# Optimization experiments

Hardware: AMD Instinct MI355X
Metric: run time of the kernel (lower is better)

The kernel has to match this reference:

```python
import jax, jax.numpy as jnp
import numpy as np

B, C, K, V, S = 16384, 1024, 128, 256, 6
HM, HG, M = 512, 384, 1024
LB = 2
GATE_DIM = C + K + 2 * V + 5  # 1669
CADENCE = 8.0
TEMP = 0.25
REFRESH_T, SPAWN_T, PROMOTE_T, RETIRE_T = 0.55, 0.60, 0.50, 0.15
DECAY = 0.995
EPS_N = 1e-6


def _mlp(x, W1, b1, W2, b2):
    return jax.nn.gelu(x @ W1 + b1, approximate=False) @ W2 + b2


def _l2norm(x):
    n = jnp.linalg.norm(x, axis=-1, keepdims=True)
    return x / jnp.maximum(n, EPS_N)


def setup_inputs():
    key = jax.random.key(0)
    ks = jax.random.split(key, 16)
    p = lambda k, sh: (0.02 * jax.random.normal(k, sh)).astype(jnp.float32)
    return {
        "context": jax.random.normal(ks[0], (B, C), jnp.float32),
        "ledger_bias": jax.random.normal(ks[1], (B, LB), jnp.float32),
        "keys": jax.random.normal(ks[2], (B, S, K), jnp.float32),
        "values": jax.random.normal(ks[3], (B, S, V), jnp.float32),
        "confidence": jax.random.uniform(ks[4], (B, S, 1), jnp.float32),
        "age": 16.0 * jax.random.uniform(ks[5], (B, S, 1), jnp.float32),
        "alive": (jax.random.uniform(ks[6], (B, S, 1)) > 0.3).astype(jnp.float32),
        "Wk1": p(ks[7], (C, HM)), "bk1": jnp.zeros(HM, jnp.float32),
        "Wk2": p(ks[8], (HM, K)), "bk2": jnp.zeros(K, jnp.float32),
        "Wv1": p(ks[9], (C, HM)), "bv1": jnp.zeros(HM, jnp.float32),
        "Wv2": p(ks[10], (HM, V)), "bv2": jnp.zeros(V, jnp.float32),
        "Wg1": p(ks[11], (4, GATE_DIM, HG)), "bg1": jnp.zeros((4, HG), jnp.float32),
        "Wg2": p(ks[12], (4, HG, 1)), "bg2": jnp.zeros((4, 1), jnp.float32),
        "Wsum": p(ks[13], (V, M)), "bsum": jnp.zeros(M, jnp.float32),
        "g_ln": jnp.ones(M, jnp.float32), "b_ln": jnp.zeros(M, jnp.float32),
    }


def _forward(context, ledger_bias, keys, values, confidence, age, alive,
             Wk1, bk1, Wk2, bk2, Wv1, bv1, Wv2, bv2,
             Wg1, bg1, Wg2, bg2, Wsum, bsum, g_ln, b_ln):
    cand_key = _l2norm(_mlp(context, Wk1, bk1, Wk2, bk2))   # [B,K]
    cand_val = _mlp(context, Wv1, bv1, Wv2, bv2)            # [B,V]
    # --- slot match: cosine similarity over live slots, gather best ---
    live = alive[..., 0] > 0                                # [B,S]
    safe_keys = _l2norm(keys + (1.0 - alive) * 1e-4)
    scores = jnp.einsum("bd,bsd->bs", cand_key, safe_keys)
    scores = jnp.where(live, scores, -1e4)
    has_live = jnp.any(live, axis=1, keepdims=True)         # [B,1]
    best_score = jnp.where(has_live, scores.max(axis=1, keepdims=True), 0.0)
    best_index = jnp.where(has_live, jnp.argmax(scores, axis=1, keepdims=True), 0)
    matched_val = jnp.take_along_axis(values, best_index[:, :, None], axis=1)[:, 0]
    matched_age = jnp.take_along_axis(age, best_index[:, :, None], axis=1)[:, 0]
    cadence_prior = jax.nn.sigmoid((matched_age - CADENCE) / CADENCE)
    surprise = 1.0 - best_score
    feats = jnp.concatenate([context, cand_key, cand_val, matched_val,
                             best_score, cadence_prior, surprise, ledger_bias], axis=-1)
    # --- four gate MLPs fused into one batched einsum ---
    h = jax.nn.gelu(jnp.einsum("bf,gfh->bgh", feats, Wg1) + bg1, approximate=False)
    probs = jax.nn.sigmoid(jnp.einsum("bgh,gho->bgo", h, Wg2) + bg2)[:, :, 0]  # [B,4]
    refresh_p, spawn_p, promote_p, retire_p = (probs[:, i:i + 1] for i in range(4))
    # --- soft masks (hard=False path) ---
    has_live_f = alive.max(axis=1)                          # [B,1]
    t = max(TEMP, 1e-4)
    refresh_raw = jax.nn.sigmoid((refresh_p - REFRESH_T) / t) * has_live_f
    spawn_raw = jax.nn.sigmoid((spawn_p - SPAWN_T) / t)
    denom = 1.0 + refresh_raw + spawn_raw
    refresh = refresh_raw / denom
    spawn = spawn_raw / denom
    promote = jax.nn.sigmoid((promote_p - PROMOTE_T) / t)
    retire = jax.nn.sigmoid((retire_p - RETIRE_T) / t)
    # --- spawn slot selection ---
    inactive = (alive[..., 0] < 0.5).astype(jnp.float32)
    has_inactive = inactive.max(axis=1, keepdims=True) > 0.5
    inactive_choice = jnp.argmax(inactive, axis=1, keepdims=True)
    utility = (confidence - 0.01 * age)[..., 0]
    utility = jnp.where(best_index == jnp.arange(S)[None, :], 1e4, utility)
    spawn_index = jnp.where(has_inactive, inactive_choice,
                            jnp.argmin(utility, axis=1, keepdims=True))
    # --- masked scatter update into slot memory ---
    match_hot = jax.nn.one_hot(best_index[:, 0], S, dtype=keys.dtype)[:, :, None]
    spawn_hot = jax.nn.one_hot(spawn_index[:, 0], S, dtype=keys.dtype)[:, :, None]
    refresh_slot = match_hot * refresh[:, None, :]
    spawn_slot = spawn_hot * spawn[:, None, :]
    retire_slot = match_hot * retire[:, None, :]
    write = jnp.clip(refresh_slot + spawn_slot, 0.0, 1.0)
    keys_n = keys * (1.0 - write) + write * cand_key[:, None, :]
    values_n = values * (1.0 - write) + write * cand_val[:, None, :]
    conf_n = (confidence * DECAY * (1.0 - write) + write) * (1.0 - retire_slot)
    age_n = (age + alive) * (1.0 - write)
    alive_n = jnp.clip(alive * (1.0 - retire_slot) + write, 0.0, 1.0)
    # --- confidence-weighted summary + promoted memory token ---
    w = alive_n * conf_n
    summary = (values_n * w).sum(axis=1) / (w.sum(axis=1) + EPS_N)  # [B,V]
    z = summary @ Wsum + bsum
    mu = z.mean(axis=-1, keepdims=True)
    var = ((z - mu) ** 2).mean(axis=-1, keepdims=True)
    promoted = promote * (((z - mu) / jnp.sqrt(var + 1e-5)) * g_ln + b_ln)
    return promoted, summary, keys_n, values_n, conf_n, age_n, alive_n


def reference(context, ledger_bias, keys, values, confidence, age, alive,
              Wk1, bk1, Wk2, bk2, Wv1, bv1, Wv2, bv2,
              Wg1, bg1, Wg2, bg2, Wsum, bsum, g_ln, b_ln):
    return _forward(context, ledger_bias, keys, values, confidence, age, alive,
                    Wk1, bk1, Wk2, bk2, Wv1, bv1, Wv2, bv2,
                    Wg1, bg1, Wg2, bg2, Wsum, bsum, g_ln, b_ln)
```

## Files before the change

kernel.cpp:

```cpp
#include <hip/hip_runtime.h>
#include <math.h>

static constexpr int Bsz  = 16384;
static constexpr int Cdim = 1024;
static constexpr int Kdim = 128;
static constexpr int Vdim = 256;
static constexpr int HMd  = 512;
static constexpr int GOUTd= 1536;
static constexpr int GDIM = 1669;
static constexpr int GPAD = 1728;
static constexpr int F2D  = 704;
static constexpr int Mdim = 1024;
static constexpr float TAU = 2e-3f;

typedef __attribute__((ext_vector_type(8))) _Float16 f16x8;
typedef __attribute__((ext_vector_type(4))) _Float16 f16x4;
typedef __attribute__((ext_vector_type(4))) float f32x4;

__device__ __forceinline__ float sigm(float x){ return 1.0f/(1.0f+__expf(-x)); }
__device__ __forceinline__ float gelu(float x){
    float y = 0.70710678118654752440f * x;
    float a = fabsf(y);
    float t1 = __builtin_amdgcn_rcpf(fmaf(0.3275911f, a, 1.0f));
    float p = t1*fmaf(t1, fmaf(t1, fmaf(t1, fmaf(t1, 1.061405429f, -1.453152027f),
                                         1.421413741f), -0.284496736f), 0.254829592f);
    float e = __expf(-a*a);
    float er = fmaf(-p, e, 1.0f);
    er = (y < 0.0f) ? -er : er;
    return 0.5f*x*(1.0f+er);
}
__device__ __forceinline__ ushort f2h(float f){
    return __builtin_bit_cast(ushort, (_Float16)f);
}


__global__ __launch_bounds__(256) void k_zero(int* p){ if (threadIdx.x==0) *p = 0; }

__global__ __launch_bounds__(256) void k_cat(float* __restrict__ dst,
        const float* __restrict__ a, const float* __restrict__ b, int na, int ntot){
    int i = blockIdx.x*256 + threadIdx.x;
    if (i >= ntot) return;
    dst[i] = (i < na) ? a[i] : b[i-na];
}

__global__ __launch_bounds__(256) void k_wt(const float* __restrict__ W,
                                            ushort* __restrict__ Wt, int K, int N){
    __shared__ float tile[64][65];
    int n0 = blockIdx.x*64, k0 = blockIdx.y*64;
    int tx = threadIdx.x & 63, ty = threadIdx.x >> 6;
    #pragma unroll
    for (int i=0;i<64;i+=4)
        tile[ty+i][tx] = W[(size_t)(k0+ty+i)*N + n0 + tx];
    __syncthreads();
    #pragma unroll
    for (int i=0;i<64;i+=4)
        Wt[(size_t)(n0+ty+i)*K + k0 + tx] = f2h(tile[tx][ty+i]);
}

__global__ __launch_bounds__(256) void k_wg1t(const float* __restrict__ Wg1,
                                              ushort* __restrict__ Wt){
    __shared__ float tile[64][65];
    int g = blockIdx.z;
    int h0 = blockIdx.x*64, f0 = blockIdx.y*64;
    int tx = threadIdx.x & 63, ty = threadIdx.x >> 6;
    #pragma unroll
    for (int i=0;i<64;i+=4){
        int f = f0+ty+i;
        tile[ty+i][tx] = (f < GDIM) ? Wg1[((size_t)g*GDIM+f)*384 + h0+tx] : 0.0f;
    }
    __syncthreads();
    #pragma unroll
    for (int i=0;i<64;i+=4)
        Wt[((size_t)(g*384 + h0+ty+i))*GPAD + f0+tx] = f2h(tile[tx][ty+i]);
}

__global__ __launch_bounds__(256) void k_cvt(const float* __restrict__ x,
                                             ushort* __restrict__ y, size_t n4){
    size_t i = (size_t)blockIdx.x*256 + threadIdx.x;
    if (i >= n4) return;
    float4 v = ((const float4*)x)[i];
    ushort4 o = { f2h(v.x), f2h(v.y), f2h(v.z), f2h(v.w) };
    ((ushort4*)y)[i] = o;
}

__device__ __forceinline__ void gload_lds16(const void* g, void* l){
    typedef __attribute__((address_space(1))) const unsigned gu32;
    typedef __attribute__((address_space(3))) unsigned lu32;
    __builtin_amdgcn_global_load_lds((gu32*)(unsigned long long)g,
                                     (lu32*)(unsigned)(unsigned long long)l,
                                     16, 0, 0);
}

template<int ACT, int OUTM, int SRC, int NX>
__global__ __launch_bounds__(512, 4) void k_mgemm(const ushort* __restrict__ A,
        const ushort* __restrict__ A2, const ushort* __restrict__ Bt,
        const float* __restrict__ bias, const float* __restrict__ Wg2,
        void* __restrict__ Cout, int K, int lda){
    __shared__ alignas(16) ushort lds[24576];
    ushort* As = lds;
    ushort* Bs = lds + 16384;
    int t = threadIdx.x;
    int l = t & 63, wv = t >> 6;
    int wrow = wv >> 1, wcol = wv & 1;
    int nwg = NX * (int)gridDim.y;
    int orig = (int)blockIdx.y * NX + (int)blockIdx.x;
    int qq = nwg >> 3, rr = nwg & 7;
    int xcd = orig & 7, loc = orig >> 3;
    int wgid = (xcd < rr ? xcd*(qq+1) : rr*(qq+1) + (xcd-rr)*qq) + loc;
    int bx = wgid % NX;
    int by = wgid / NX;
    size_t row0 = (size_t)by * 256;
    int col0 = bx * 128;
    constexpr int N = NX*128;
    f32x4 acc[4][4] = {};
    int lrow = l >> 3;
    int lc8  = (l & 7) ^ lrow;

    for (int k0 = 0; k0 < K; k0 += 64){
        const ushort* Ag; size_t astr; int koff;
        if (SRC == 1){
            if (k0 < 1024){ Ag = A;  astr = 1024; koff = k0; }
            else          { Ag = A2; astr = F2D;  koff = k0 - 1024; }
        } else if (SRC == 2){
            Ag = A; astr = (size_t)lda; koff = k0 + (bx ? 512 : 0);
        } else { Ag = A; astr = (size_t)lda; koff = k0; }
        #pragma unroll
        for (int i = 0; i < 4; ++i){
            int ch = wv*4 + i;
            int r  = ch*8 + lrow;
            gload_lds16(Ag + (row0 + r)*astr + koff + lc8*8, As + ch*512);
        }
        #pragma unroll
        for (int i = 0; i < 2; ++i){
            int ch = wv*2 + i;
            int r  = ch*8 + lrow;
            gload_lds16(Bt + (size_t)(col0 + r)*K + k0 + lc8*8, Bs + ch*512);
        }
        __syncthreads();
        #pragma unroll
        for (int kk = 0; kk < 2; ++kk){
            f16x8 af[4], bfr[4];
            int j8 = kk*4 + (l >> 4);
            #pragma unroll
            for (int m = 0; m < 4; ++m){
                int row = wrow*64 + m*16 + (l & 15);
                int c16 = j8 ^ (row & 7);
                af[m] = *(const f16x8*)(const void*)(As + row*64 + c16*8);
            }
            #pragma unroll
            for (int n = 0; n < 4; ++n){
                int rowb = wcol*64 + n*16 + (l & 15);
                int c16 = j8 ^ (rowb & 7);
                bfr[n] = *(const f16x8*)(const void*)(Bs + rowb*64 + c16*8);
            }
            #pragma unroll
            for (int m = 0; m < 4; ++m)
                #pragma unroll
                for (int n = 0; n < 4; ++n)
                    acc[m][n] = __builtin_amdgcn_mfma_f32_16x16x32_f16(af[m], bfr[n], acc[m][n], 0, 0, 0);
        }
        __syncthreads();
    }
    int q = l >> 4, cf = l & 15;
    if (OUTM == 2){
        float* sacc = (float*)lds;
        if (t < 256) sacc[t] = 0.f;
        __syncthreads();
        #pragma unroll
        for (int m = 0; m < 4; ++m){
            #pragma unroll
            for (int i = 0; i < 4; ++i){
                float v = 0.f;
                #pragma unroll
                for (int n = 0; n < 4; ++n){
                    int col = col0 + wcol*64 + n*16 + cf;
                    float z = acc[m][n][i] + bias[col];
                    v += gelu(z) * Wg2[col];
                }
                atomicAdd(&sacc[wrow*64 + m*16 + q*4 + i], v);
            }
        }
        __syncthreads();
        if (t < 256) ((float*)Cout)[(row0 + t)*NX + bx] = sacc[t];
    } else {
        #pragma unroll
        for (int m = 0; m < 4; ++m){
            #pragma unroll
            for (int n = 0; n < 4; ++n){
                int col = col0 + wcol*64 + n*16 + cf;
                float bv = bias[col];
                #pragma unroll
                for (int i = 0; i < 4; ++i){
                    size_t r = row0 + wrow*64 + m*16 + q*4 + i;
                    float v = acc[m][n][i] + bv;
                    if (ACT == 1) v = gelu(v);
                    if (OUTM == 1) ((ushort*)Cout)[r*N + col] = f2h(v);
                    else           ((float*) Cout)[r*N + col] = v;
                }
            }
        }
    }
}

template<int ACT>
__global__ __launch_bounds__(256) void k_gemm_dyn(const float* __restrict__ A,
                                                  const float* __restrict__ W,
                                                  const float* __restrict__ bias,
                                                  float* __restrict__ C,
                                                  const int* __restrict__ cntp,
                                                  int N, int K){
    int M = (*cntp + 63) & ~63;
    size_t row0 = (size_t)blockIdx.y * 64;
    if ((int)row0 >= M) return;
    __shared__ float As[32][68];
    __shared__ float Ws[32][64];
    int t  = threadIdx.x;
    int tx = t & 15, ty = t >> 4;
    int col0 = blockIdx.x * 64;
    float acc[4][4] = {};
    int ra = t >> 3;
    int ca = (t & 7) << 2;
    int rw = t >> 4;
    int cw = (t & 15) << 2;
    for (int k0 = 0; k0 < K; k0 += 32){
        float4 a0 = *(const float4*)(A + (row0 + ra)*K + k0 + ca);
        float4 a1 = *(const float4*)(A + (row0 + ra + 32)*K + k0 + ca);
        float4 w0 = *(const float4*)(W + (size_t)(k0 + rw)*N + col0 + cw);
        float4 w1 = *(const float4*)(W + (size_t)(k0 + rw + 16)*N + col0 + cw);
        As[ca+0][ra] = a0.x; As[ca+1][ra] = a0.y; As[ca+2][ra] = a0.z; As[ca+3][ra] = a0.w;
        As[ca+0][ra+32] = a1.x; As[ca+1][ra+32] = a1.y; As[ca+2][ra+32] = a1.z; As[ca+3][ra+32] = a1.w;
        *(float4*)&Ws[rw][cw]    = w0;
        *(float4*)&Ws[rw+16][cw] = w1;
        __syncthreads();
        #pragma unroll
        for (int kk = 0; kk < 32; ++kk){
            float4 av = *(const float4*)&As[kk][ty*4];
            float4 wv = *(const float4*)&Ws[kk][tx*4];
            float a4[4] = {av.x, av.y, av.z, av.w};
            float w4[4] = {wv.x, wv.y, wv.z, wv.w};
            #pragma unroll
            for (int i=0;i<4;i++)
                #pragma unroll
                for (int j=0;j<4;j++)
                    acc[i][j] = fmaf(a4[i], w4[j], acc[i][j]);
        }
        __syncthreads();
    }
    #pragma unroll
    for (int i=0;i<4;i++){
        size_t r = row0 + ty*4 + i;
        #pragma unroll
        for (int j=0;j<4;j++){
            int c = col0 + tx*4 + j;
            float v = acc[i][j] + bias[c];
            if (ACT == 1) v = gelu(v);
            C[r*N + c] = v;
        }
    }
}

__global__ __launch_bounds__(256) void k_gather(const float* __restrict__ ctx,
        const int* __restrict__ flaglist, const int* __restrict__ flagcnt,
        float* __restrict__ fctx, int b0){
    int i = (blockIdx.x<<2) + (threadIdx.x>>6);
    int lane = threadIdx.x & 63;
    int cnt = *flagcnt;
    int cntpad = (cnt + 63) & ~63;
    if (i >= cntpad) return;
    float4* dst = (float4*)(fctx + (size_t)i*1024);
    if (i < cnt){
        const float4* src = (const float4*)(ctx + ((size_t)b0 + flaglist[i])*1024);
        #pragma unroll
        for (int j=0;j<4;j++) dst[lane + 64*j] = src[lane + 64*j];
    } else {
        float4 z = {0.f,0.f,0.f,0.f};
        #pragma unroll
        for (int j=0;j<4;j++) dst[lane + 64*j] = z;
    }
}

__global__ __launch_bounds__(256) void k_fixapply(const float* __restrict__ fck,
        const float* __restrict__ keys, const float* __restrict__ values,
        const float* __restrict__ age,  const float* __restrict__ alive,
        float* __restrict__ ckc, ushort* __restrict__ feats2, int* __restrict__ bidx,
        const int* __restrict__ flagcnt, const int* __restrict__ flaglist, int b0){
    int i = (blockIdx.x<<2) + (threadIdx.x>>6);
    int lane = threadIdx.x & 63;
    if (i >= *flagcnt) return;
    int w = flaglist[i];
    size_t b = (size_t)b0 + w;
    float2 c2 = ((const float2*)(fck + (size_t)i*128))[lane];
    float ss = c2.x*c2.x + c2.y*c2.y;
    #pragma unroll
    for (int o=32;o;o>>=1) ss += __shfl_xor(ss,o);
    float inv = 1.0f / fmaxf(sqrtf(ss), 1e-6f);
    float2 cc; cc.x = c2.x*inv; cc.y = c2.y*inv;
    ((float2*)(ckc + (size_t)w*128))[lane] = cc;
    ushort* f2 = feats2 + (size_t)w*F2D;
    { ushort2 o = { f2h(cc.x), f2h(cc.y) };
      ((ushort2*)f2)[lane] = o; }
    float s1v = -1e30f; int bi = 0; int anylive = 0;
    #pragma unroll
    for (int s=0;s<6;s++){
        float a = alive[b*6+s];
        float2 k2 = ((const float2*)(keys + (b*6+s)*128))[lane];
        float ks = k2.x*k2.x + k2.y*k2.y;
        float dt = cc.x*k2.x + cc.y*k2.y;
        #pragma unroll
        for (int o=32;o;o>>=1){ ks += __shfl_xor(ks,o); dt += __shfl_xor(dt,o); }
        float sc;
        if (a > 0.0f){ sc = dt / fmaxf(sqrtf(ks), 1e-6f); anylive = 1; }
        else sc = -1e4f;
        if (sc > s1v){ s1v = sc; bi = s; }
    }
    int bis = anylive ? bi : 0;
    float bsc = anylive ? s1v : 0.0f;
    float4 mv = ((const float4*)(values + (b*6+bis)*256))[lane];
    ushort4 mo = { f2h(mv.x), f2h(mv.y), f2h(mv.z), f2h(mv.w) };
    ((ushort4*)(f2+384))[lane] = mo;
    if (lane == 0){
        bidx[w] = bis;
        float mage = age[b*6 + bis];
        f2[640] = f2h(bsc);
        f2[641] = f2h(sigm((mage - 8.0f)*0.125f));
        f2[642] = f2h(1.0f - bsc);
    }
}

__global__ __launch_bounds__(256) void k_feats(
        const float* __restrict__ ledger, const float* __restrict__ keys,
        const float* __restrict__ values, const float* __restrict__ age,
        const float* __restrict__ alive,  const float* __restrict__ ckv,
        float* __restrict__ ckc, ushort* __restrict__ feats2,
        int* __restrict__ bidx, int* __restrict__ flagcnt, int* __restrict__ flaglist,
        int b0){
    int w = (blockIdx.x<<2) + (threadIdx.x>>6);
    int lane = threadIdx.x & 63;
    size_t b = (size_t)b0 + w;
    const float* ckr = ckv + (size_t)w*384;
    float2 cr2 = ((const float2*)ckr)[lane];
    float ssc = cr2.x*cr2.x + cr2.y*cr2.y;
    #pragma unroll
    for (int o=32;o;o>>=1) ssc += __shfl_xor(ssc,o);
    float invc = 1.0f / fmaxf(sqrtf(ssc), 1e-6f);
    float2 cc; cc.x = cr2.x*invc; cc.y = cr2.y*invc;
    ((float2*)(ckc + (size_t)w*128))[lane] = cc;
    float s1v = -1e30f, s2v = -1e30f; int bi = 0; int anylive = 0;
    #pragma unroll
    for (int s=0;s<6;s++){
        float a = alive[b*6+s];
        float2 k2 = ((const float2*)(keys + (b*6+s)*128))[lane];
        float ss = k2.x*k2.x + k2.y*k2.y;
        float dt = cc.x*k2.x + cc.y*k2.y;
        #pragma unroll
        for (int o=32;o;o>>=1){ ss += __shfl_xor(ss,o); dt += __shfl_xor(dt,o); }
        float sc;
        if (a > 0.0f){ sc = dt / fmaxf(sqrtf(ss), 1e-6f); anylive = 1; }
        else sc = -1e4f;
        if (sc > s1v){ s2v = s1v; s1v = sc; bi = s; }
        else if (sc > s2v) s2v = sc;
    }
    float best_score = anylive ? s1v : 0.0f;
    int bis = anylive ? bi : 0;
    if (lane == 0 && (s1v - s2v) < TAU){
        int pos = atomicAdd(flagcnt, 1);
        flaglist[pos] = w;
    }
    float4 mv = ((const float4*)(values + (b*6+bis)*256))[lane];
    float mage = age[b*6+bis];
    float cad = sigm((mage - 8.0f)*0.125f);
    ushort* f2 = feats2 + (size_t)w*F2D;
    { ushort2 o = { f2h(cc.x), f2h(cc.y) };
      ((ushort2*)f2)[lane] = o; }
    { float4 v = ((const float4*)(ckr+128))[lane];
      ushort4 o = { f2h(v.x), f2h(v.y), f2h(v.z), f2h(v.w) };
      ((ushort4*)(f2+128))[lane] = o; }
    { ushort4 o = { f2h(mv.x), f2h(mv.y), f2h(mv.z), f2h(mv.w) };
      ((ushort4*)(f2+384))[lane] = o; }
    if (lane == 0){
        f2[640] = f2h(best_score);
        f2[641] = f2h(cad);
        f2[642] = f2h(1.0f - best_score);
        f2[643] = f2h(ledger[b*2]);
        f2[644] = f2h(ledger[b*2+1]);
        bidx[w] = bis;
    }
    if (lane < GPAD - GDIM) f2[645+lane] = 0;
}

__global__ __launch_bounds__(256) void k_update(const float* __restrict__ keys,
        const float* __restrict__ values, const float* __restrict__ conf,
        const float* __restrict__ age,    const float* __restrict__ alive,
        const float* __restrict__ ckC,    const float* __restrict__ ckv,
        const float* __restrict__ part,   const float* __restrict__ bg2,
        const int* __restrict__ bidx,
        float* __restrict__ probsC,
        float* __restrict__ o_keys, float* __restrict__ o_vals,
        float* __restrict__ o_conf, float* __restrict__ o_age,
        float* __restrict__ o_aliv, float* __restrict__ o_sum,
        ushort* __restrict__ o_sumb, int b0){
    int w = (blockIdx.x<<2) + (threadIdx.x>>6);
    int lane = threadIdx.x & 63;
    size_t b = (size_t)b0 + w;
    const float* pp = part + (size_t)w*12;
    float pb[4];
    #pragma unroll
    for (int g=0; g<4; ++g)
        pb[g] = sigm(pp[3*g] + pp[3*g+1] + pp[3*g+2] + bg2[g]);
    if (lane < 4) probsC[w*4 + lane] = pb[lane];
    float rp = pb[0], sp = pb[1], tp = pb[3];
    float al[6], cf[6], ag[6];
    float hl = 0.f;
    #pragma unroll
    for (int s=0;s<6;s++){
        al[s]=alive[b*6+s]; cf[s]=conf[b*6+s]; ag[s]=age[b*6+s];
        hl = fmaxf(hl, al[s]);
    }
    float rr = hl * sigm((rp-0.55f)*4.0f);
    float sr = sigm((sp-0.60f)*4.0f);
    float den = 1.0f + rr + sr;
    float refresh = rr/den, spawn = sr/den;
    float retire = sigm((tp-0.15f)*4.0f);
    int bi = bidx[w];
    int ic = -1;
    #pragma unroll
    for (int s=5;s>=0;s--) if (al[s] < 0.5f) ic = s;
    int si;
    if (ic >= 0) si = ic;
    else {
        float bu = 1e30f; int am = 0;
        #pragma unroll
        for (int s=0;s<6;s++){
            float u = (s == bi) ? 1e4f : (cf[s] - 0.01f*ag[s]);
            if (u < bu){ bu = u; am = s; }
        }
        si = am;
    }
    float2 cc  = ((const float2*)(ckC + (size_t)w*128))[lane];
    float4 cvv = ((const float4*)(ckv + (size_t)w*384 + 128))[lane];
    float s0=0,s1=0,s2=0,s3=0, wsum=0;
    #pragma unroll
    for (int s=0;s<6;s++){
        float wr = refresh*(s==bi ? 1.0f:0.0f) + spawn*(s==si ? 1.0f:0.0f);
        wr = fminf(wr, 1.0f);
        float rs = (s==bi) ? retire : 0.0f;
        float om = 1.0f - wr;
        float2 k2 = ((const float2*)(keys + (b*6+s)*128))[lane];
        float2 kn; kn.x = k2.x*om + wr*cc.x; kn.y = k2.y*om + wr*cc.y;
        ((float2*)(o_keys + (b*6+s)*128))[lane] = kn;
        float4 vv = ((const float4*)(values + (b*6+s)*256))[lane];
        float4 vn;
        vn.x = vv.x*om + wr*cvv.x; vn.y = vv.y*om + wr*cvv.y;
        vn.z = vv.z*om + wr*cvv.z; vn.w = vv.w*om + wr*cvv.w;
        ((float4*)(o_vals + (b*6+s)*256))[lane] = vn;
        float cn  = (cf[s]*0.995f*om + wr) * (1.0f - rs);
        float an  = fminf(fmaxf(al[s]*(1.0f - rs) + wr, 0.0f), 1.0f);
        float agn = (ag[s] + al[s]) * om;
        float wgt = an * cn;
        wsum += wgt;
        s0 += vn.x*wgt; s1 += vn.y*wgt; s2 += vn.z*wgt; s3 += vn.w*wgt;
        if (lane == s){ o_conf[b*6+s] = cn; o_age[b*6+s] = agn; o_aliv[b*6+s] = an; }
    }
    float inv = 1.0f/(wsum + 1e-6f);
    float4 sm; sm.x = s0*inv; sm.y = s1*inv; sm.z = s2*inv; sm.w = s3*inv;
    ((float4*)(o_sum + b*256))[lane] = sm;
    ushort4 sb = { f2h(sm.x), f2h(sm.y), f2h(sm.z), f2h(sm.w) };
    ((ushort4*)(o_sumb + (size_t)w*256))[lane] = sb;
}

__global__ __launch_bounds__(256) void k_ln(const ushort* __restrict__ z,
        const float* __restrict__ probs, const float* __restrict__ g_ln,
        const float* __restrict__ b_ln,  float* __restrict__ o_prom, int b0){
    int w = blockIdx.x; int t = threadIdx.x;
    int lane = t & 63, wid = t >> 6;
    f16x4 hv = ((const f16x4*)(z + (size_t)w*1024))[t];
    float v0 = (float)hv[0], v1 = (float)hv[1], v2 = (float)hv[2], v3 = (float)hv[3];
    float s = v0+v1+v2+v3;
    #pragma unroll
    for (int o=32;o;o>>=1) s += __shfl_xor(s,o);
    __shared__ float red[4];
    if (lane==0) red[wid] = s;
    __syncthreads();
    float mu = (red[0]+red[1]+red[2]+red[3]) * (1.0f/1024.0f);
    float d0=v0-mu, d1=v1-mu, d2=v2-mu, d3=v3-mu;
    float ss = d0*d0+d1*d1+d2*d2+d3*d3;
    #pragma unroll
    for (int o=32;o;o>>=1) ss += __shfl_xor(ss,o);
    __syncthreads();
    if (lane==0) red[wid] = ss;
    __syncthreads();
    float var = (red[0]+red[1]+red[2]+red[3]) * (1.0f/1024.0f);
    float rstd = 1.0f / sqrtf(var + 1e-5f);
    float pm = sigm((probs[w*4+2]-0.50f)*4.0f);
    float4 g  = ((const float4*)g_ln)[t];
    float4 bb = ((const float4*)b_ln)[t];
    float4 o;
    o.x = pm*(d0*rstd*g.x + bb.x);
    o.y = pm*(d1*rstd*g.y + bb.y);
    o.z = pm*(d2*rstd*g.z + bb.z);
    o.w = pm*(d3*rstd*g.w + bb.w);
    ((float4*)(o_prom + ((size_t)b0 + w)*1024))[t] = o;
}

extern "C" void kernel_launch(void* const* d_in, const int* in_sizes, int n_in,
                              void* d_out, int out_size, void* d_ws, size_t ws_size,
                              hipStream_t stream){
    const float* ctx    = (const float*)d_in[0];
    const float* ledger = (const float*)d_in[1];
    const float* keys   = (const float*)d_in[2];
    const float* values = (const float*)d_in[3];
    const float* conf   = (const float*)d_in[4];
    const float* age    = (const float*)d_in[5];
    const float* alive  = (const float*)d_in[6];
    const float* Wk1 = (const float*)d_in[7];  const float* bk1 = (const float*)d_in[8];
    const float* Wk2 = (const float*)d_in[9];  const float* bk2 = (const float*)d_in[10];
    const float* Wv1 = (const float*)d_in[11]; const float* bv1 = (const float*)d_in[12];
    const float* Wv2 = (const float*)d_in[13]; const float* bv2 = (const float*)d_in[14];
    const float* Wg1 = (const float*)d_in[15]; const float* bg1 = (const float*)d_in[16];
    const float* Wg2 = (const float*)d_in[17]; const float* bg2 = (const float*)d_in[18];
    const float* Wsum= (const float*)d_in[19]; const float* bsum= (const float*)d_in[20];
    const float* g_ln= (const float*)d_in[21]; const float* b_ln= (const float*)d_in[22];

    float* out   = (float*)d_out;
    float* o_prom= out;
    float* o_sum = o_prom + (size_t)Bsz*Mdim;
    float* o_keys= o_sum  + (size_t)Bsz*Vdim;
    float* o_vals= o_keys + (size_t)Bsz*6*Kdim;
    float* o_conf= o_vals + (size_t)Bsz*6*Vdim;
    float* o_age = o_conf + (size_t)Bsz*6;
    float* o_aliv= o_age  + (size_t)Bsz*6;

    char* p = (char*)d_ws;
    auto alloc = [&](size_t bytes)->char*{
        char* r = p; p += (bytes + 255) & ~(size_t)255; return r;
    };
    ushort* ctxh  = (ushort*)alloc((size_t)Bsz*Cdim*2);
    ushort* W1m   = (ushort*)alloc((size_t)1024*Cdim*2);
    ushort* W2m   = (ushort*)alloc((size_t)384*HMd*2);
    ushort* Wg1tt = (ushort*)alloc((size_t)GOUTd*GPAD*2);
    ushort* Wsumt = (ushort*)alloc((size_t)Mdim*Vdim*2);
    float*  biasm1= (float*) alloc(1024*4);
    float*  biasm2= (float*) alloc(384*4);
    size_t fixed = (size_t)(p - (char*)d_ws);
    size_t per_row = 2048 + 1536 + 512 + 1408 + 48 + 4096 + 512 + 16
                   + 4 + 4 + 2048 + 512 + 128;
    int CB = 16384;
    while (CB > 256 && fixed + (size_t)CB*per_row + 16384 > ws_size) CB >>= 1;
    ushort* H      = (ushort*)alloc((size_t)CB*1024*2);
    float*  ckv    = (float*) alloc((size_t)CB*384*4);
    float*  ckc    = (float*) alloc((size_t)CB*Kdim*4);
    ushort* feats2 = (ushort*)alloc((size_t)CB*F2D*2);
    float*  part   = (float*) alloc((size_t)CB*12*4);
    float*  zbuf   = (float*) alloc((size_t)CB*Mdim*4);
    ushort* sumb   = (ushort*)alloc((size_t)CB*Vdim*2);
    float*  probsC = (float*) alloc((size_t)CB*4*4);
    int*    bidxC  = (int*)   alloc((size_t)CB*4);
    int*    flagl  = (int*)   alloc((size_t)CB*4);
    int*    flagc  = (int*)   alloc(256);
    float*  fH     = (float*) alloc((size_t)CB*HMd*4);
    float*  fck    = (float*) alloc((size_t)CB*Kdim*4);
    float*  fctx   = zbuf;
    ushort* zh     = (ushort*)zbuf;

    dim3 blk(256);
    dim3 blk512(512);
    k_cvt<<<(int)(((size_t)Bsz*Cdim/4 + 255)/256), blk, 0, stream>>>(ctx, ctxh, (size_t)Bsz*Cdim/4);
    k_wt<<<dim3(HMd/64,  Cdim/64), blk, 0, stream>>>(Wk1, W1m,             Cdim, HMd);
    k_wt<<<dim3(HMd/64,  Cdim/64), blk, 0, stream>>>(Wv1, W1m + 512*Cdim,  Cdim, HMd);
    k_wt<<<dim3(Kdim/64, HMd/64),  blk, 0, stream>>>(Wk2, W2m,             HMd, Kdim);
    k_wt<<<dim3(Vdim/64, HMd/64),  blk, 0, stream>>>(Wv2, W2m + 128*HMd,   HMd, Vdim);
    k_wt<<<dim3(Mdim/64, Vdim/64), blk, 0, stream>>>(Wsum, Wsumt, Vdim, Mdim);
    k_wg1t<<<dim3(384/64, GPAD/64, 4), blk, 0, stream>>>(Wg1, Wg1tt);
    k_cat<<<(1024+255)/256, blk, 0, stream>>>(biasm1, bk1, bv1, 512, 1024);
    k_cat<<<(384+255)/256,  blk, 0, stream>>>(biasm2, bk2, bv2, 128, 384);

    for (int b0 = 0; b0 < Bsz; b0 += CB){
        k_zero<<<1, blk, 0, stream>>>(flagc);
        k_mgemm<1,1,0,8><<<dim3(8, CB/256), blk512, 0, stream>>>(
            ctxh + (size_t)b0*Cdim, nullptr, W1m, biasm1, nullptr, H, Cdim, Cdim);
        k_mgemm<0,0,2,3><<<dim3(3, CB/256), blk512, 0, stream>>>(
            H, nullptr, W2m, biasm2, nullptr, ckv, HMd, 1024);
        k_feats<<<CB/4, blk, 0, stream>>>(ledger, keys, values, age, alive,
                                          ckv, ckc, feats2, bidxC, flagc, flagl, b0);
        k_gather<<<CB/4, blk, 0, stream>>>(ctx, flagl, flagc, fctx, b0);
        k_gemm_dyn<1><<<dim3(HMd/64,  CB/64), blk, 0, stream>>>(fctx, Wk1, bk1, fH,  flagc, HMd,  Cdim);
        k_gemm_dyn<0><<<dim3(Kdim/64, CB/64), blk, 0, stream>>>(fH,   Wk2, bk2, fck, flagc, Kdim, HMd);
        k_fixapply<<<CB/4, blk, 0, stream>>>(fck, keys, values, age, alive,
                                             ckc, feats2, bidxC, flagc, flagl, b0);
        k_mgemm<0,2,1,12><<<dim3(12, CB/256), blk512, 0, stream>>>(
            ctxh + (size_t)b0*Cdim, feats2, Wg1tt, bg1, Wg2, part, GPAD, 0);
        k_update<<<CB/4, blk, 0, stream>>>(keys, values, conf, age, alive, ckc, ckv,
                                           part, bg2, bidxC, probsC,
                                           o_keys, o_vals, o_conf, o_age, o_aliv,
                                           o_sum, sumb, b0);
        k_mgemm<0,1,0,8><<<dim3(8, CB/256), blk512, 0, stream>>>(
            sumb, nullptr, Wsumt, bsum, nullptr, zh, Vdim, Vdim);
        k_ln<<<CB, blk, 0, stream>>>(zh, probsC, g_ln, b_ln, o_prom, b0);
    }
}
```

Baseline: 448.9 us.

## Use FP8 MFMA for the context part of the gate GEMM

```diff
diff --git a/kernel.cpp b/kernel.cpp
--- a/kernel.cpp
+++ b/kernel.cpp
@@ -32,6 +32,12 @@
 __device__ __forceinline__ ushort f2h(float f){
     return __builtin_bit_cast(ushort, (_Float16)f);
 }
+__device__ __forceinline__ unsigned f2q4(float a, float b, float c, float d){
+    int v = 0;
+    v = __builtin_amdgcn_cvt_pk_fp8_f32(a, b, v, false);
+    v = __builtin_amdgcn_cvt_pk_fp8_f32(c, d, v, true);
+    return (unsigned)v;
+}
 
 
 __global__ __launch_bounds__(256) void k_zero(int* p){ if (threadIdx.x==0) *p = 0; }
@@ -57,30 +63,51 @@
         Wt[(size_t)(n0+ty+i)*K + k0 + tx] = f2h(tile[tx][ty+i]);
 }
 
-__global__ __launch_bounds__(256) void k_wg1t(const float* __restrict__ Wg1,
-                                              ushort* __restrict__ Wt){
-    __shared__ float tile[64][65];
-    int g = blockIdx.z;
-    int h0 = blockIdx.x*64, f0 = blockIdx.y*64;
-    int tx = threadIdx.x & 63, ty = threadIdx.x >> 6;
-    #pragma unroll
-    for (int i=0;i<64;i+=4){
-        int f = f0+ty+i;
-        tile[ty+i][tx] = (f < GDIM) ? Wg1[((size_t)g*GDIM+f)*384 + h0+tx] : 0.0f;
-    }
-    __syncthreads();
-    #pragma unroll
-    for (int i=0;i<64;i+=4)
-        Wt[((size_t)(g*384 + h0+ty+i))*GPAD + f0+tx] = f2h(tile[tx][ty+i]);
-}
-
-__global__ __launch_bounds__(256) void k_cvt(const float* __restrict__ x,
-                                             ushort* __restrict__ y, size_t n4){
-    size_t i = (size_t)blockIdx.x*256 + threadIdx.x;
-    if (i >= n4) return;
-    float4 v = ((const float4*)x)[i];
-    ushort4 o = { f2h(v.x), f2h(v.y), f2h(v.z), f2h(v.w) };
-    ((ushort4*)y)[i] = o;
+__global__ __launch_bounds__(256) void k_wg1t8(const float* __restrict__ Wg1,
+                                               unsigned char* __restrict__ B8){
+    int idx = blockIdx.x*256 + threadIdx.x;
+    if (idx >= 1536*128) return;
+    int n = idx >> 7, ur = idx & 127;
+    int g = n / 384, h = n - g*384;
+    int f0 = ur*8;
+    float v[8];
+    #pragma unroll
+    for (int j=0;j<8;j++) v[j] = Wg1[((size_t)g*GDIM + f0 + j)*384 + h];
+    unsigned q0 = f2q4(v[0],v[1],v[2],v[3]), q1 = f2q4(v[4],v[5],v[6],v[7]);
+    int seg = ur >> 4, ul = ur & 15;
+    size_t pos = (size_t)n*1024 + seg*128 + (size_t)(ul ^ (n&7))*8;
+    ((unsigned*)(B8+pos))[0] = q0;
+    ((unsigned*)(B8+pos))[1] = q1;
+}
+
+__global__ __launch_bounds__(256) void k_wg1tf(const float* __restrict__ Wg1,
+                                               ushort* __restrict__ Wt){
+    int idx = blockIdx.x*256 + threadIdx.x;
+    if (idx >= 1536*704) return;
+    int n = idx / 704, k = idx - n*704;
+    int g = n / 384, h = n - g*384;
+    int f = 1024 + k;
+    float v = (f < GDIM) ? Wg1[((size_t)g*GDIM + f)*384 + h] : 0.0f;
+    Wt[(size_t)n*704 + k] = f2h(v);
+}
+
+__global__ __launch_bounds__(256) void k_cvt8(const float* __restrict__ x,
+        ushort* __restrict__ yh, unsigned char* __restrict__ y8, int nunits){
+    int i = blockIdx.x*256 + threadIdx.x;
+    if (i >= nunits) return;
+    const float4* src = (const float4*)(x + (size_t)i*8);
+    float4 v0 = src[0], v1 = src[1];
+    ushort4 h0 = { f2h(v0.x), f2h(v0.y), f2h(v0.z), f2h(v0.w) };
+    ushort4 h1 = { f2h(v1.x), f2h(v1.y), f2h(v1.z), f2h(v1.w) };
+    ((ushort4*)yh)[(size_t)i*2]   = h0;
+    ((ushort4*)yh)[(size_t)i*2+1] = h1;
+    unsigned q0 = f2q4(v0.x,v0.y,v0.z,v0.w), q1 = f2q4(v1.x,v1.y,v1.z,v1.w);
+    int row = i >> 7;
+    int ur  = i & 127;
+    int seg = ur >> 4, ul = ur & 15;
+    size_t pos = (size_t)row*1024 + seg*128 + (size_t)(ul ^ (row&7))*8;
+    ((unsigned*)(y8+pos))[0] = q0;
+    ((unsigned*)(y8+pos))[1] = q1;
 }
 
 __device__ __forceinline__ void gload_lds16(const void* g, void* l){
@@ -118,10 +145,7 @@
 
     for (int k0 = 0; k0 < K; k0 += 64){
         const ushort* Ag; size_t astr; int koff;
-        if (SRC == 1){
-            if (k0 < 1024){ Ag = A;  astr = 1024; koff = k0; }
-            else          { Ag = A2; astr = F2D;  koff = k0 - 1024; }
-        } else if (SRC == 2){
+        if (SRC == 2){
             Ag = A; astr = (size_t)lda; koff = k0 + (bx ? 512 : 0);
         } else { Ag = A; astr = (size_t)lda; koff = k0; }
         #pragma unroll
@@ -162,44 +186,147 @@
         __syncthreads();
     }
     int q = l >> 4, cf = l & 15;
-    if (OUTM == 2){
-        float* sacc = (float*)lds;
-        if (t < 256) sacc[t] = 0.f;
+    #pragma unroll
+    for (int m = 0; m < 4; ++m){
+        #pragma unroll
+        for (int n = 0; n < 4; ++n){
+            int col = col0 + wcol*64 + n*16 + cf;
+            float bv = bias[col];
+            #pragma unroll
+            for (int i = 0; i < 4; ++i){
+                size_t r = row0 + wrow*64 + m*16 + q*4 + i;
+                float v = acc[m][n][i] + bv;
+                if (ACT == 1) v = gelu(v);
+                if (OUTM == 1) ((ushort*)Cout)[r*N + col] = f2h(v);
+                else           ((float*) Cout)[r*N + col] = v;
+            }
+        }
+    }
+}
+
+__global__ __launch_bounds__(512, 4) void k_ggemm(const unsigned char* __restrict__ A8,
+        const ushort* __restrict__ Af, const unsigned char* __restrict__ B8,
+        const ushort* __restrict__ Bf, const float* __restrict__ bias,
+        const float* __restrict__ Wg2, float* __restrict__ part){
+    __shared__ alignas(16) unsigned char lds[49152];
+    unsigned char* As8 = lds;
+    unsigned char* Bs8 = lds + 32768;
+    ushort* As16 = (ushort*)lds;
+    ushort* Bs16 = (ushort*)(lds + 32768);
+    int t = threadIdx.x, l = t & 63, wv = t >> 6;
+    int wrow = wv >> 1, wcol = wv & 1;
+    constexpr int NX = 12;
+    int nwg = NX * (int)gridDim.y;
+    int orig = (int)blockIdx.y * NX + (int)blockIdx.x;
+    int qq = nwg >> 3, rr = nwg & 7;
+    int xcd = orig & 7, loc = orig >> 3;
+    int wgid = (xcd < rr ? xcd*(qq+1) : rr*(qq+1) + (xcd-rr)*qq) + loc;
+    int bx = wgid % NX;
+    int by = wgid / NX;
+    size_t row0 = (size_t)by * 256;
+    int col0 = bx * 128;
+    f32x4 acc[4][4] = {};
+    int lrow = l >> 3;
+
+    for (int kt = 0; kt < 8; ++kt){
+        int k0 = kt << 7;
+        #pragma unroll
+        for (int i = 0; i < 4; ++i){
+            int ch = wv*4 + i;
+            int r  = ch*8 + lrow;
+            gload_lds16(A8 + (row0 + r)*1024 + k0 + (l&7)*16, As8 + ch*1024);
+        }
+        #pragma unroll
+        for (int i = 0; i < 2; ++i){
+            int ch = wv*2 + i;
+            int r  = ch*8 + lrow;
+            gload_lds16(B8 + (size_t)(col0 + r)*1024 + k0 + (l&7)*16, Bs8 + ch*1024);
+        }
         __syncthreads();
         #pragma unroll
-        for (int m = 0; m < 4; ++m){
-            #pragma unroll
-            for (int i = 0; i < 4; ++i){
-                float v = 0.f;
+        for (int kk = 0; kk < 4; ++kk){
+            long a8[4], b8[4];
+            int j8 = (l >> 4) + kk*4;
+            #pragma unroll
+            for (int m = 0; m < 4; ++m){
+                int row = wrow*64 + m*16 + (l & 15);
+                int u = j8 ^ (row & 7);
+                a8[m] = *(const long*)(const void*)(As8 + row*128 + u*8);
+            }
+            #pragma unroll
+            for (int n = 0; n < 4; ++n){
+                int col = wcol*64 + n*16 + (l & 15);
+                int u = j8 ^ (col & 7);
+                b8[n] = *(const long*)(const void*)(Bs8 + col*128 + u*8);
+            }
+            #pragma unroll
+            for (int m = 0; m < 4; ++m)
                 #pragma unroll
-                for (int n = 0; n < 4; ++n){
-                    int col = col0 + wcol*64 + n*16 + cf;
-                    float z = acc[m][n][i] + bias[col];
-                    v += gelu(z) * Wg2[col];
-                }
-                atomicAdd(&sacc[wrow*64 + m*16 + q*4 + i], v);
+                for (int n = 0; n < 4; ++n)
+                    acc[m][n] = __builtin_amdgcn_mfma_f32_16x16x32_fp8_fp8(a8[m], b8[n], acc[m][n], 0, 0, 0);
+        }
+        __syncthreads();
+    }
+    int lc8 = (l & 7) ^ lrow;
+    for (int tt = 0; tt < 11; ++tt){
+        int k0 = tt << 6;
+        #pragma unroll
+        for (int i = 0; i < 4; ++i){
+            int ch = wv*4 + i;
+            int r  = ch*8 + lrow;
+            gload_lds16(Af + (row0 + r)*(size_t)F2D + k0 + lc8*8, As16 + ch*512);
+        }
+        #pragma unroll
+        for (int i = 0; i < 2; ++i){
+            int ch = wv*2 + i;
+            int r  = ch*8 + lrow;
+            gload_lds16(Bf + (size_t)(col0 + r)*F2D + k0 + lc8*8, Bs16 + ch*512);
+        }
+        __syncthreads();
+        #pragma unroll
+        for (int kk = 0; kk < 2; ++kk){
+            f16x8 af[4], bfr[4];
+            int j8 = kk*4 + (l >> 4);
+            #pragma unroll
+            for (int m = 0; m < 4; ++m){
+                int row = wrow*64 + m*16 + (l & 15);
+                int c16 = j8 ^ (row & 7);
+                af[m] = *(const f16x8*)(const void*)(As16 + row*64 + c16*8);
             }
+            #pragma unroll
+            for (int n = 0; n < 4; ++n){
+                int col = wcol*64 + n*16 + (l & 15);
+                int c16 = j8 ^ (col & 7);
+                bfr[n] = *(const f16x8*)(const void*)(Bs16 + col*64 + c16*8);
+            }
+            #pragma unroll
+            for (int m = 0; m < 4; ++m)
+                #pragma unroll
+                for (int n = 0; n < 4; ++n)
+                    acc[m][n] = __builtin_amdgcn_mfma_f32_16x16x32_f16(af[m], bfr[n], acc[m][n], 0, 0, 0);
         }
         __syncthreads();
-        if (t < 256) ((float*)Cout)[(row0 + t)*NX + bx] = sacc[t];
-    } else {
-        #pragma unroll
-        for (int m = 0; m < 4; ++m){
+    }
+    int q = l >> 4, cf = l & 15;
+    float* sacc = (float*)lds;
+    if (t < 256) sacc[t] = 0.f;
+    __syncthreads();
+    #pragma unroll
+    for (int m = 0; m < 4; ++m){
+        #pragma unroll
+        for (int i = 0; i < 4; ++i){
+            float v = 0.f;
             #pragma unroll
             for (int n = 0; n < 4; ++n){
                 int col = col0 + wcol*64 + n*16 + cf;
-                float bv = bias[col];
-                #pragma unroll
-                for (int i = 0; i < 4; ++i){
-                    size_t r = row0 + wrow*64 + m*16 + q*4 + i;
-                    float v = acc[m][n][i] + bv;
-                    if (ACT == 1) v = gelu(v);
-                    if (OUTM == 1) ((ushort*)Cout)[r*N + col] = f2h(v);
-                    else           ((float*) Cout)[r*N + col] = v;
-                }
+                float z = acc[m][n][i] + bias[col];
+                v += gelu(z) * Wg2[col];
             }
-        }
-    }
+            atomicAdd(&sacc[wrow*64 + m*16 + q*4 + i], v);
+        }
+    }
+    __syncthreads();
+    if (t < 256) part[(row0 + t)*NX + bx] = sacc[t];
 }
 
 template<int ACT>
@@ -535,9 +662,11 @@
         char* r = p; p += (bytes + 255) & ~(size_t)255; return r;
     };
     ushort* ctxh  = (ushort*)alloc((size_t)Bsz*Cdim*2);
+    unsigned char* ctx8 = (unsigned char*)alloc((size_t)Bsz*Cdim);
     ushort* W1m   = (ushort*)alloc((size_t)1024*Cdim*2);
     ushort* W2m   = (ushort*)alloc((size_t)384*HMd*2);
-    ushort* Wg1tt = (ushort*)alloc((size_t)GOUTd*GPAD*2);
+    unsigned char* Wg1t8 = (unsigned char*)alloc((size_t)GOUTd*1024);
+    ushort* Wg1tf = (ushort*)alloc((size_t)GOUTd*F2D*2);
     ushort* Wsumt = (ushort*)alloc((size_t)Mdim*Vdim*2);
     float*  biasm1= (float*) alloc(1024*4);
     float*  biasm2= (float*) alloc(384*4);
@@ -564,13 +693,15 @@
 
     dim3 blk(256);
     dim3 blk512(512);
-    k_cvt<<<(int)(((size_t)Bsz*Cdim/4 + 255)/256), blk, 0, stream>>>(ctx, ctxh, (size_t)Bsz*Cdim/4);
+    k_cvt8<<<(int)(((size_t)Bsz*Cdim/8 + 255)/256), blk, 0, stream>>>(
+        ctx, ctxh, ctx8, (int)((size_t)Bsz*Cdim/8));
     k_wt<<<dim3(HMd/64,  Cdim/64), blk, 0, stream>>>(Wk1, W1m,             Cdim, HMd);
     k_wt<<<dim3(HMd/64,  Cdim/64), blk, 0, stream>>>(Wv1, W1m + 512*Cdim,  Cdim, HMd);
     k_wt<<<dim3(Kdim/64, HMd/64),  blk, 0, stream>>>(Wk2, W2m,             HMd, Kdim);
     k_wt<<<dim3(Vdim/64, HMd/64),  blk, 0, stream>>>(Wv2, W2m + 128*HMd,   HMd, Vdim);
     k_wt<<<dim3(Mdim/64, Vdim/64), blk, 0, stream>>>(Wsum, Wsumt, Vdim, Mdim);
-    k_wg1t<<<dim3(384/64, GPAD/64, 4), blk, 0, stream>>>(Wg1, Wg1tt);
+    k_wg1t8<<<(1536*128 + 255)/256, blk, 0, stream>>>(Wg1, Wg1t8);
+    k_wg1tf<<<(1536*704 + 255)/256, blk, 0, stream>>>(Wg1, Wg1tf);
     k_cat<<<(1024+255)/256, blk, 0, stream>>>(biasm1, bk1, bv1, 512, 1024);
     k_cat<<<(384+255)/256,  blk, 0, stream>>>(biasm2, bk2, bv2, 128, 384);
 
@@ -587,8 +718,8 @@
         k_gemm_dyn<0><<<dim3(Kdim/64, CB/64), blk, 0, stream>>>(fH,   Wk2, bk2, fck, flagc, Kdim, HMd);
         k_fixapply<<<CB/4, blk, 0, stream>>>(fck, keys, values, age, alive,
                                              ckc, feats2, bidxC, flagc, flagl, b0);
-        k_mgemm<0,2,1,12><<<dim3(12, CB/256), blk512, 0, stream>>>(
-            ctxh + (size_t)b0*Cdim, feats2, Wg1tt, bg1, Wg2, part, GPAD, 0);
+        k_ggemm<<<dim3(12, CB/256), blk512, 0, stream>>>(
+            ctx8 + (size_t)b0*Cdim, feats2, Wg1t8, Wg1tf, bg1, Wg2, part);
         k_update<<<CB/4, blk, 0, stream>>>(keys, values, conf, age, alive, ckc, ckv,
                                            part, bg2, bidxC, probsC,
                                            o_keys, o_vals, o_conf, o_age, o_aliv,
```

After: 450.9 us. Within noise of the previous version (+0.4%).
